# Kernel optimization log

Measured on AMD Instinct MI355X. Metric: run time of the kernel, lower is better.

Reference implementation:

```python
import jax, jax.numpy as jnp
import numpy as np

D_MODEL = 1024
N_HEAD = 16
D_H = D_MODEL // N_HEAD


def setup_inputs() -> dict:
    key = jax.random.key(0)
    ks = jax.random.split(key, 5)
    scale = 1.0 / np.sqrt(D_MODEL)
    x = jax.random.normal(ks[0], (4, 2048, D_MODEL), dtype=jnp.float32)
    # torch nn.Linear weights: shape (out_features, in_features)
    W_qkv = jax.random.uniform(ks[1], (3 * D_MODEL, D_MODEL), dtype=jnp.float32, minval=-scale, maxval=scale)
    b_qkv = jax.random.uniform(ks[2], (3 * D_MODEL,), dtype=jnp.float32, minval=-scale, maxval=scale)
    W_o = jax.random.uniform(ks[3], (D_MODEL, D_MODEL), dtype=jnp.float32, minval=-scale, maxval=scale)
    b_o = jax.random.uniform(ks[4], (D_MODEL,), dtype=jnp.float32, minval=-scale, maxval=scale)
    return {"x": x, "W_qkv": W_qkv, "b_qkv": b_qkv, "W_o": W_o, "b_o": b_o}


def reference(x, W_qkv, b_qkv, W_o, b_o):
    B, S, D = x.shape
    qkv = jnp.einsum('bsd,ed->bse', x, W_qkv) + b_qkv  # [B,S,3D]
    q, k, v = jnp.split(qkv, 3, axis=-1)
    # [B,H,S,d_h]
    q = q.reshape(B, S, N_HEAD, D_H).transpose(0, 2, 1, 3)
    k = k.reshape(B, S, N_HEAD, D_H).transpose(0, 2, 1, 3)
    v = v.reshape(B, S, N_HEAD, D_H).transpose(0, 2, 1, 3)
    sim = jnp.einsum('bhqd,bhkd->bhqk', q, k) / jnp.sqrt(jnp.float32(D_H))
    neg_inf = jnp.finfo(sim.dtype).min
    causal = jnp.tril(jnp.ones((S, S), dtype=bool))
    sim = jnp.where(causal[None, None], sim, neg_inf)
    attn = jax.nn.softmax(sim, axis=-1)
    out = jnp.einsum('bhqk,bhkd->bhqd', attn, v)  # [B,H,S,d_h]
    out = out.transpose(0, 2, 1, 3).reshape(B, S, D)
    return jnp.einsum('bsd,ed->bse', out, W_o) + b_o
```

## Files before the change

### kernel.cpp

```cpp
#include <hip/hip_runtime.h>

#define D_MODEL 1024
#define S_LEN   2048
#define BATCH   4
#define NH      16
#define DH      64
#define M_ROWS  (BATCH * S_LEN)

typedef __attribute__((ext_vector_type(8))) short short8;
typedef __attribute__((ext_vector_type(4))) float floatx4;
typedef unsigned short ushort_t;
typedef __attribute__((ext_vector_type(4))) ushort_t ushortx4;

__device__ __forceinline__ ushort_t f2bf(float f) {
    union { float f; unsigned u; } v; v.f = f;
    unsigned r = v.u + 0x7FFFu + ((v.u >> 16) & 1u);
    return (ushort_t)(r >> 16);
}

__device__ __forceinline__ int pack2(float lo, float hi) {
    return (int)__builtin_amdgcn_perm(__float_as_uint(hi), __float_as_uint(lo), 0x07060302u);
}

__device__ __forceinline__ void async_copy16(const ushort_t* g, ushort_t* l) {
    __builtin_amdgcn_global_load_lds(
        (const __attribute__((address_space(1))) void*)g,
        (__attribute__((address_space(3))) void*)l,
        16, 0, 0);
}

#define N0 (M_ROWS * D_MODEL)
#define N1 (3 * D_MODEL * D_MODEL)
#define N2 (D_MODEL * D_MODEL)
#define NQUADS ((N0 + N1 + N2) / 4)

__global__ __launch_bounds__(256)
void cvt_f32_bf16(const float* __restrict__ s0, const float* __restrict__ s1,
                  const float* __restrict__ s2, ushort_t* __restrict__ d0,
                  ushort_t* __restrict__ d1, ushort_t* __restrict__ d2)
{
    const int q = blockIdx.x * 256 + threadIdx.x;
    if (q >= NQUADS) return;
    const float* s; ushort_t* d; int e;
    if (q < N0 / 4)            { s = s0; d = d0; e = q * 4; }
    else if (q < (N0 + N1) / 4){ s = s1; d = d1; e = q * 4 - N0; }
    else                       { s = s2; d = d2; e = q * 4 - N0 - N1; }
    const float4 v = *(const float4*)&s[e];
    ushortx4 o;
    o[0] = f2bf(v.x); o[1] = f2bf(v.y); o[2] = f2bf(v.z); o[3] = f2bf(v.w);
    *(ushortx4*)&d[e] = o;
}

template<bool F32OUT, bool VSPLIT>
__global__ __launch_bounds__(256)
void gemm_bt_bias(const ushort_t* __restrict__ A, const ushort_t* __restrict__ B,
                  const float* __restrict__ bias, void* __restrict__ Cv,
                  ushort_t* __restrict__ vt, int M, int N, int K)
{
    constexpr int BK = 64;
    constexpr float C2 = 0.18033688011112042f;
    __shared__ ushort_t As[128][BK];
    __shared__ ushort_t Bs[128][BK];

    const int tid  = threadIdx.x;
    const int lane = tid & 63;
    const int wave = tid >> 6;
    const int quad = lane >> 4;
    const int l16  = lane & 15;
    const int bm   = blockIdx.y * 128;
    const int bn   = blockIdx.x * 128;
    const int wm   = (wave & 1) * 64;
    const int wn   = (wave >> 1) * 64;

    floatx4 acc[4][4] = {};

    const int l8r = lane >> 3;
    const int c8  = lane & 7;
    const int swz = l16 & 7;

    for (int k0 = 0; k0 < K; k0 += BK) {
        __syncthreads();
        #pragma unroll
        for (int i = wave; i < 16; i += 4) {
            const int row = i * 8 + l8r;
            const int cc  = (c8 ^ l8r) * 8;
            async_copy16(&A[(size_t)(bm + row) * K + k0 + cc], &As[i * 8][0]);
            async_copy16(&B[(size_t)(bn + row) * K + k0 + cc], &Bs[i * 8][0]);
        }
        __syncthreads();

        #pragma unroll
        for (int h = 0; h < 2; h++) {
            short8 af[4], bfr[4];
            #pragma unroll
            for (int i = 0; i < 4; i++)
                af[i]  = *(const short8*)&As[wm + i * 16 + l16][((h * 4 + quad) ^ swz) * 8];
            #pragma unroll
            for (int i = 0; i < 4; i++)
                bfr[i] = *(const short8*)&Bs[wn + i * 16 + l16][((h * 4 + quad) ^ swz) * 8];

            #pragma unroll
            for (int mi = 0; mi < 4; mi++)
                #pragma unroll
                for (int ni = 0; ni < 4; ni++)
                    acc[mi][ni] = __builtin_amdgcn_mfma_f32_16x16x32_bf16(af[mi], bfr[ni], acc[mi][ni], 0, 0, 0);
        }
    }

    #pragma unroll
    for (int ni = 0; ni < 4; ni++) {
        const int col = bn + wn + ni * 16 + l16;
        const float bv = bias[col];
        #pragma unroll
        for (int mi = 0; mi < 4; mi++)
            #pragma unroll
            for (int r = 0; r < 4; r++) {
                const int row = bm + wm + mi * 16 + quad * 4 + r;
                const float val = acc[mi][ni][r] + bv;
                if (VSPLIT) {
                    if (col < 2 * D_MODEL) {
                        const float vv = (col < D_MODEL) ? val * C2 : val;
                        ((ushort_t*)Cv)[(size_t)row * 2048 + col] = f2bf(vv);
                    } else {
                        const int vcol = col - 2 * D_MODEL;
                        const int h = vcol >> 6, dh = vcol & 63;
                        const int b = row >> 11, s = row & 2047;
                        const int sp = (s & ~63) | ((s & 15) << 2) | ((s >> 4) & 3);
                        vt[(((size_t)(b * NH + h)) * DH + dh) * S_LEN + sp] = f2bf(val);
                    }
                } else if (F32OUT) {
                    ((float*)Cv)[(size_t)row * N + col] = val;
                } else {
                    ((ushort_t*)Cv)[(size_t)row * N + col] = f2bf(val);
                }
            }
    }
}

#define BKV 64

struct TileState {
    short8  qf[2];
    floatx4 o[4];
    float   l[4];
};

__device__ __forceinline__ void attn_tile(
    const ushort_t (*__restrict__ Ks)[DH], const ushort_t (*__restrict__ Vs)[BKV],
    ushort_t (*__restrict__ Psw)[BKV + 4], TileState& st, bool diag,
    int wave, int quad, int l16, int swz, short8 ones)
{
    floatx4 sc[4];
    #pragma unroll
    for (int ns = 0; ns < 4; ns++) {
        const short8 kf0 = *(const short8*)&Ks[ns * 16 + l16][(quad ^ swz) * 8];
        const short8 kf1 = *(const short8*)&Ks[ns * 16 + l16][((4 + quad) ^ swz) * 8];
        floatx4 z = {};
        z = __builtin_amdgcn_mfma_f32_16x16x32_bf16(st.qf[0], kf0, z, 0, 0, 0);
        z = __builtin_amdgcn_mfma_f32_16x16x32_bf16(st.qf[1], kf1, z, 0, 0, 0);
        sc[ns] = z;
    }

    #pragma unroll
    for (int r = 0; r < 4; r++) {
        const int qloc = wave * 16 + quad * 4 + r;
        float p[4];
        #pragma unroll
        for (int ns = 0; ns < 4; ns++) {
            float v = sc[ns][r];
            if (diag) {
                const int kj = ns * 16 + l16;
                v = (kj <= qloc) ? v : -1e30f;
            }
            p[ns] = __builtin_amdgcn_exp2f(v);
        }
        int2 w;
        w.x = pack2(p[0], p[1]);
        w.y = pack2(p[2], p[3]);
        *(int2*)&Psw[quad * 4 + r][l16 * 4] = w;
    }

    short8 pf[2];
    #pragma unroll
    for (int c = 0; c < 2; c++)
        pf[c] = *(const short8*)&Psw[l16][c * 32 + quad * 8];

    floatx4 racc = {};
    racc = __builtin_amdgcn_mfma_f32_16x16x32_bf16(pf[0], ones, racc, 0, 0, 0);
    racc = __builtin_amdgcn_mfma_f32_16x16x32_bf16(pf[1], ones, racc, 0, 0, 0);

    #pragma unroll
    for (int r = 0; r < 4; r++)
        st.l[r] += racc[r];

    #pragma unroll
    for (int d = 0; d < 4; d++) {
        #pragma unroll
        for (int c = 0; c < 2; c++) {
            const short8 vf = *(const short8*)&Vs[d * 16 + l16][((c * 4 + quad) ^ swz) * 8];
            st.o[d] = __builtin_amdgcn_mfma_f32_16x16x32_bf16(pf[c], vf, st.o[d], 0, 0, 0);
        }
    }
}

__global__ __launch_bounds__(256, 4)
void attn_causal(const ushort_t* __restrict__ qk, const ushort_t* __restrict__ vt,
                 ushort_t* __restrict__ out)
{
    __shared__ ushort_t Ks[BKV][DH];
    __shared__ ushort_t Vs[DH][BKV];
    __shared__ ushort_t Ps[4][16][BKV + 4];

    const int tid  = threadIdx.x;
    const int lane = tid & 63;
    const int wave = tid >> 6;
    const int quad = lane >> 4;
    const int l16  = lane & 15;
    const int l8r  = lane >> 3;
    const int c8   = lane & 7;
    const int swz  = l16 & 7;

    const int qa = blockIdx.x;
    const int qb = 31 - qa;
    const int bh = blockIdx.y;
    const int b  = bh >> 4;
    const int h  = bh & 15;

    const size_t qkbase = (size_t)b * S_LEN * 2048;
    const ushort_t* kg = qk + qkbase + D_MODEL + h * DH;
    const ushort_t* vg = vt + (size_t)(b * NH + h) * DH * S_LEN;

    TileState sa, sb;
    #pragma unroll
    for (int r = 0; r < 4; r++) { sa.l[r] = 0.f; sb.l[r] = 0.f; }
    #pragma unroll
    for (int d = 0; d < 4; d++) { sa.o[d] = (floatx4){}; sb.o[d] = (floatx4){}; }

    {
        const ushort_t* qpa = qk + qkbase + (size_t)(qa * 64 + wave * 16 + l16) * 2048 + h * DH;
        sa.qf[0] = *(const short8*)(qpa + quad * 8);
        sa.qf[1] = *(const short8*)(qpa + 32 + quad * 8);
        const ushort_t* qpb = qk + qkbase + (size_t)(qb * 64 + wave * 16 + l16) * 2048 + h * DH;
        sb.qf[0] = *(const short8*)(qpb + quad * 8);
        sb.qf[1] = *(const short8*)(qpb + 32 + quad * 8);
    }

    short8 ones;
    #pragma unroll
    for (int j = 0; j < 8; j++) ones[j] = (short)0x3F80;

    for (int t = 0; t <= qb; t++) {
        const int kb = t * BKV;
        __syncthreads();
        #pragma unroll
        for (int i = wave; i < 8; i += 4) {
            const int row = i * 8 + l8r;
            const int cc  = (c8 ^ l8r) * 8;
            async_copy16(&kg[(size_t)(kb + row) * 2048 + cc], &Ks[i * 8][0]);
            async_copy16(&vg[(size_t)row * S_LEN + kb + cc], &Vs[i * 8][0]);
        }
        __syncthreads();

        if (t <= qa) attn_tile(Ks, Vs, Ps[wave], sa, t == qa, wave, quad, l16, swz, ones);
        attn_tile(Ks, Vs, Ps[wave], sb, t == qb, wave, quad, l16, swz, ones);
    }

    #pragma unroll
    for (int r = 0; r < 4; r++) {
        const float inva = 1.0f / sa.l[r];
        const float invb = 1.0f / sb.l[r];
        const int ra = qa * 64 + wave * 16 + quad * 4 + r;
        const int rb = qb * 64 + wave * 16 + quad * 4 + r;
        #pragma unroll
        for (int d = 0; d < 4; d++) {
            out[(size_t)(b * S_LEN + ra) * D_MODEL + h * DH + d * 16 + l16] = f2bf(sa.o[d][r] * inva);
            out[(size_t)(b * S_LEN + rb) * D_MODEL + h * DH + d * 16 + l16] = f2bf(sb.o[d][r] * invb);
        }
    }
}

extern "C" void kernel_launch(void* const* d_in, const int* in_sizes, int n_in,
                              void* d_out, int out_size, void* d_ws, size_t ws_size,
                              hipStream_t stream)
{
    const float* x    = (const float*)d_in[0];
    const float* Wqkv = (const float*)d_in[1];
    const float* bqkv = (const float*)d_in[2];
    const float* Wo   = (const float*)d_in[3];
    const float* bo   = (const float*)d_in[4];
    float* out = (float*)d_out;

    ushort_t* xb    = (ushort_t*)d_ws;
    ushort_t* wqkvb = xb + N0;
    ushort_t* wob   = wqkvb + N1;
    ushort_t* qkbuf = wob + N2;
    ushort_t* vtbuf = qkbuf + (size_t)M_ROWS * 2048;
    ushort_t* att   = vtbuf + (size_t)BATCH * NH * DH * S_LEN;

    dim3 blk(256);
    cvt_f32_bf16<<<dim3((NQUADS + 255) / 256), blk, 0, stream>>>(x, Wqkv, Wo, xb, wqkvb, wob);
    gemm_bt_bias<false, true><<<dim3((3 * D_MODEL) / 128, M_ROWS / 128), blk, 0, stream>>>(
        xb, wqkvb, bqkv, qkbuf, vtbuf, M_ROWS, 3 * D_MODEL, D_MODEL);
    attn_causal<<<dim3(16, BATCH * NH), blk, 0, stream>>>(qkbuf, vtbuf, att);
    gemm_bt_bias<true, false><<<dim3(D_MODEL / 128, M_ROWS / 128), blk, 0, stream>>>(
        att, wob, bo, out, nullptr, M_ROWS, D_MODEL, D_MODEL);
}
```

Baseline: 279.4 us.

## Double-buffer K/V tiles in attention and XOR-swizzle the P scratch buffer

The attention loop now keeps two shared-memory K/V buffers. It issues the async copy for the next key tile before computing on the current one, which removes one barrier per iteration and overlaps global loads with MFMA work. The padded P staging buffer is replaced with an unpadded 64-wide layout that uses an XOR swizzle to avoid LDS bank conflicts. The cost is higher LDS use per block (roughly 40KB), which may limit occupancy at four blocks per CU.

```diff
diff --git a/kernel.cpp b/kernel.cpp
--- a/kernel.cpp
+++ b/kernel.cpp
@@ -147,7 +147,7 @@
 
 __device__ __forceinline__ void attn_tile(
     const ushort_t (*__restrict__ Ks)[DH], const ushort_t (*__restrict__ Vs)[BKV],
-    ushort_t (*__restrict__ Psw)[BKV + 4], TileState& st, bool diag,
+    ushort_t* __restrict__ Psw, TileState& st, bool diag,
     int wave, int quad, int l16, int swz, short8 ones)
 {
     floatx4 sc[4];
@@ -177,13 +177,14 @@
         int2 w;
         w.x = pack2(p[0], p[1]);
         w.y = pack2(p[2], p[3]);
-        *(int2*)&Psw[quad * 4 + r][l16 * 4] = w;
+        const int row = quad * 4 + r;
+        *(int2*)((char*)Psw + row * 128 + (((l16 >> 1) ^ (row & 7)) << 4) + ((l16 & 1) << 3)) = w;
     }
 
     short8 pf[2];
     #pragma unroll
     for (int c = 0; c < 2; c++)
-        pf[c] = *(const short8*)&Psw[l16][c * 32 + quad * 8];
+        pf[c] = *(const short8*)((const char*)Psw + l16 * 128 + ((((c << 2) | quad) ^ (l16 & 7)) << 4));
 
     floatx4 racc = {};
     racc = __builtin_amdgcn_mfma_f32_16x16x32_bf16(pf[0], ones, racc, 0, 0, 0);
@@ -203,13 +204,27 @@
     }
 }
 
+__device__ __forceinline__ void stage_tile(
+    const ushort_t* __restrict__ kg, const ushort_t* __restrict__ vg, int kb,
+    ushort_t (*__restrict__ Ksb)[DH], ushort_t (*__restrict__ Vsb)[BKV],
+    int wave, int l8r, int c8)
+{
+    #pragma unroll
+    for (int i = wave; i < 8; i += 4) {
+        const int row = i * 8 + l8r;
+        const int cc  = (c8 ^ l8r) * 8;
+        async_copy16(&kg[(size_t)(kb + row) * 2048 + cc], &Ksb[i * 8][0]);
+        async_copy16(&vg[(size_t)row * S_LEN + kb + cc], &Vsb[i * 8][0]);
+    }
+}
+
 __global__ __launch_bounds__(256, 4)
 void attn_causal(const ushort_t* __restrict__ qk, const ushort_t* __restrict__ vt,
                  ushort_t* __restrict__ out)
 {
-    __shared__ ushort_t Ks[BKV][DH];
-    __shared__ ushort_t Vs[DH][BKV];
-    __shared__ ushort_t Ps[4][16][BKV + 4];
+    __shared__ ushort_t Ks[2][BKV][DH];
+    __shared__ ushort_t Vs[2][DH][BKV];
+    __shared__ ushort_t Ps[4][16][64];
 
     const int tid  = threadIdx.x;
     const int lane = tid & 63;
@@ -249,20 +264,17 @@
     #pragma unroll
     for (int j = 0; j < 8; j++) ones[j] = (short)0x3F80;
 
+    stage_tile(kg, vg, 0, Ks[0], Vs[0], wave, l8r, c8);
+
+    int cur = 0;
     for (int t = 0; t <= qb; t++) {
-        const int kb = t * BKV;
         __syncthreads();
-        #pragma unroll
-        for (int i = wave; i < 8; i += 4) {
-            const int row = i * 8 + l8r;
-            const int cc  = (c8 ^ l8r) * 8;
-            async_copy16(&kg[(size_t)(kb + row) * 2048 + cc], &Ks[i * 8][0]);
-            async_copy16(&vg[(size_t)row * S_LEN + kb + cc], &Vs[i * 8][0]);
-        }
-        __syncthreads();
-
-        if (t <= qa) attn_tile(Ks, Vs, Ps[wave], sa, t == qa, wave, quad, l16, swz, ones);
-        attn_tile(Ks, Vs, Ps[wave], sb, t == qb, wave, quad, l16, swz, ones);
+        if (t < qb)
+            stage_tile(kg, vg, (t + 1) * BKV, Ks[cur ^ 1], Vs[cur ^ 1], wave, l8r, c8);
+
+        if (t <= qa) attn_tile(Ks[cur], Vs[cur], &Ps[wave][0][0], sa, t == qa, wave, quad, l16, swz, ones);
+        attn_tile(Ks[cur], Vs[cur], &Ps[wave][0][0], sb, t == qb, wave, quad, l16, swz, ones);
+        cur ^= 1;
     }
 
     #pragma unroll
```

Measured after the change: 264.1 us. 5.5% less time.
